# Optimization experiments

Hardware: AMD Instinct MI355X
Metric: run time of the kernel (lower is better)

The kernel has to match this reference:

```python
import jax, jax.numpy as jnp
import numpy as np

NUM_GROUPS = 32
EPS = 1e-6
NUM_HEADS = 8
HEAD_DIM = 64


def group_norm(x, gamma, beta):
    # x: [B, C, H, W]
    B, C, H, W = x.shape
    xg = x.reshape(B, NUM_GROUPS, C // NUM_GROUPS, H, W)
    mean = xg.mean(axis=(2, 3, 4), keepdims=True)
    var = xg.var(axis=(2, 3, 4), keepdims=True)
    xn = ((xg - mean) * jax.lax.rsqrt(var + EPS)).reshape(B, C, H, W)
    return xn * gamma[None, :, None, None] + beta[None, :, None, None]


def setup_inputs() -> dict:
    key = jax.random.key(0)
    ks = jax.random.split(key, 4)
    B, C, H, W = 8, 512, 32, 32
    hid = NUM_HEADS * HEAD_DIM  # 512
    x = jax.random.normal(ks[0], (B, C, H, W), dtype=jnp.float32)
    gamma = jnp.ones((C,), dtype=jnp.float32)
    beta = jnp.zeros((C,), dtype=jnp.float32)
    w_in = jax.random.normal(ks[1], (3 * hid, C), dtype=jnp.float32) * (1.0 / np.sqrt(C))
    b_in = jnp.zeros((3 * hid,), dtype=jnp.float32)
    w_out = jax.random.normal(ks[2], (C, hid), dtype=jnp.float32) * (1.0 / np.sqrt(hid))
    b_out = jnp.zeros((C,), dtype=jnp.float32)
    return {"x": x, "gamma": gamma, "beta": beta, "w_in": w_in, "b_in": b_in,
            "w_out": w_out, "b_out": b_out}


def reference(x, gamma, beta, w_in, b_in, w_out, b_out):
    B, C, H, W = x.shape
    n, c = NUM_HEADS, HEAD_DIM
    skip = x
    h = group_norm(x, gamma, beta)
    # 1x1 conv proj_in: [B, 3*n*c, H, W]
    qkv = jnp.einsum('oc,bchw->bohw', w_in, h) + b_in[None, :, None, None]
    qkv = qkv.reshape(B, 3, n, c, H * W)
    q, k, v = qkv[:, 0], qkv[:, 1], qkv[:, 2]  # each [B, n, c, HW]
    scale = 1.0 / np.sqrt(c)
    logits = jnp.einsum('bncq,bnck->bnqk', q, k) * scale  # [B, n, HW, HW]
    w = jax.nn.softmax(logits, axis=-1)
    out = jnp.einsum('bnqk,bnck->bncq', w, v)  # [B, n, c, HW]
    out = out.reshape(B, n * c, H, W)
    out = jnp.einsum('oc,bchw->bohw', w_out, out) + b_out[None, :, None, None]
    return out + skip
```

## Files before the change

### kernel.cpp

```cpp
#include <hip/hip_runtime.h>
#include <hip/hip_bf16.h>

#define B_    8
#define C_    512
#define HW_   1024
#define NG    32
#define GCH   16
#define EPSV  1e-6f

typedef __attribute__((ext_vector_type(8))) short short8;
typedef __attribute__((ext_vector_type(4))) short short4v;
typedef __attribute__((ext_vector_type(4))) float floatx4;

static __device__ __forceinline__ short f2bs(float f) {
  return __builtin_bit_cast(short, __float2bfloat16(f));
}
static __device__ __forceinline__ short4v pack4(float a, float b, float c, float d) {
  return (short4v){f2bs(a), f2bs(b), f2bs(c), f2bs(d)};
}
#define MFMA(a, b, c) __builtin_amdgcn_mfma_f32_16x16x32_bf16((a), (b), (c), 0, 0, 0)

static __device__ __forceinline__ void glds16(const short* g, short* l) {
  __builtin_amdgcn_global_load_lds(
      (const __attribute__((address_space(1))) void*)g,
      (__attribute__((address_space(3))) void*)l, 16, 0, 0);
}

__global__ __launch_bounds__(256) void cast2_f2b(
    const float* __restrict__ s1, short* __restrict__ d1,
    const float* __restrict__ s2, short* __restrict__ d2) {
  int i = blockIdx.x * 256 + threadIdx.x;
  const float* s; short* d; int j;
  if (i < 196608) { s = s1; d = d1; j = i; }
  else            { s = s2; d = d2; j = i - 196608; }
  float4 v = reinterpret_cast<const float4*>(s)[j];
  reinterpret_cast<short4v*>(d)[j] = pack4(v.x, v.y, v.z, v.w);
}

__global__ __launch_bounds__(256) void gn_stats(
    const float* __restrict__ x, float2* __restrict__ stats) {
  int bg = blockIdx.x;
  const int n = GCH * HW_;
  const float* xp = x + (size_t)bg * n;
  int t = threadIdx.x;

  float s = 0.f, ss = 0.f;
  for (int i = t; i < n / 4; i += 256) {
    float4 v = *reinterpret_cast<const float4*>(xp + i * 4);
    s  += (v.x + v.y) + (v.z + v.w);
    ss += (v.x * v.x + v.y * v.y) + (v.z * v.z + v.w * v.w);
  }
  for (int o = 32; o > 0; o >>= 1) {
    s  += __shfl_down(s, o);
    ss += __shfl_down(ss, o);
  }
  __shared__ float rs_[4], rss_[4];
  int wid = t >> 6, lane = t & 63;
  if (lane == 0) { rs_[wid] = s; rss_[wid] = ss; }
  __syncthreads();
  if (t == 0) {
    float stot  = rs_[0] + rs_[1] + rs_[2] + rs_[3];
    float sstot = rss_[0] + rss_[1] + rss_[2] + rss_[3];
    float mean = stot / (float)n;
    float var  = sstot / (float)n - mean * mean;
    stats[bg] = make_float2(mean, rsqrtf(var + EPSV));
  }
}

__global__ __launch_bounds__(256) void gn_apply(
    const float* __restrict__ x, const float2* __restrict__ stats,
    const float* __restrict__ gamma, const float* __restrict__ beta,
    short* __restrict__ ht) {
  __shared__ float Ls[64 * 65];
  int s0 = blockIdx.x * 64, ch0 = blockIdx.y * 64, b = blockIdx.z;
  int t = threadIdx.x;

  for (int i = 0; i < 4; i++) {
    int lin = t + i * 256;
    int r = lin >> 4, c4 = lin & 15;
    int ch = ch0 + r;
    float2 st = stats[b * NG + (ch >> 4)];
    float ga = gamma[ch] * st.y;
    float be = beta[ch] - st.x * ga;
    float4 v = *reinterpret_cast<const float4*>(
        x + ((size_t)(b * C_ + ch)) * HW_ + s0 + c4 * 4);
    Ls[r * 65 + c4 * 4 + 0] = v.x * ga + be;
    Ls[r * 65 + c4 * 4 + 1] = v.y * ga + be;
    Ls[r * 65 + c4 * 4 + 2] = v.z * ga + be;
    Ls[r * 65 + c4 * 4 + 3] = v.w * ga + be;
  }
  __syncthreads();
  for (int i = 0; i < 4; i++) {
    int lin = t + i * 256;
    int sq = lin >> 4, cq = lin & 15;
    float a0 = Ls[(cq * 4 + 0) * 65 + sq];
    float a1 = Ls[(cq * 4 + 1) * 65 + sq];
    float a2 = Ls[(cq * 4 + 2) * 65 + sq];
    float a3 = Ls[(cq * 4 + 3) * 65 + sq];
    *reinterpret_cast<short4v*>(
        ht + ((size_t)b * 1024 + s0 + sq) * 512 + ch0 + cq * 4) =
        pack4(a0, a1, a2, a3);
  }
}

__global__ __launch_bounds__(256) void gemm_qkv(
    const short* __restrict__ Wb, const short* __restrict__ ht,
    const float* __restrict__ bias,
    short* __restrict__ Qt, short* __restrict__ Kt, short* __restrict__ Vn) {
  __shared__ short As[2][4096];
  __shared__ short Bs[2][4096];
  int bx = blockIdx.x, by = blockIdx.y, bb = blockIdx.z;
  int m0 = by * 128, n0 = bx * 128;
  int t = threadIdx.x;
  int w = t >> 6, lane = t & 63, n16 = lane & 15, quad = lane >> 4;
  int wm = (w >> 1) * 64, wn = (w & 1) * 64;

  const short* Wa = Wb + (size_t)(m0 + (t >> 2)) * 512 + (t & 3) * 8;
  const short* Xa = ht + (size_t)bb * 1024 * 512 +
                    (size_t)(n0 + (t >> 2)) * 512 + (t & 3) * 8;

#define STAGE(buf, kk)                                                \
  do {                                                                \
    glds16(Wa + (kk), &As[buf][t * 8]);                               \
    glds16(Wa + 64 * 512 + (kk), &As[buf][2048 + t * 8]);             \
    glds16(Xa + (kk), &Bs[buf][t * 8]);                               \
    glds16(Xa + 64 * 512 + (kk), &Bs[buf][2048 + t * 8]);             \
  } while (0)

  floatx4 acc[4][4];
  for (int i = 0; i < 4; i++)
    for (int j = 0; j < 4; j++) acc[i][j] = (floatx4){0.f, 0.f, 0.f, 0.f};

  STAGE(0, 0);
#pragma unroll 1
  for (int ks = 0; ks < 16; ks++) {
    int cur = ks & 1;
    __syncthreads();
    if (ks < 15) STAGE(cur ^ 1, (ks + 1) * 32);
    short8 a[4], b[4];
    for (int im = 0; im < 4; im++)
      a[im] = *reinterpret_cast<const short8*>(
          &As[cur][(wm + im * 16 + n16) * 32 + quad * 8]);
    for (int in = 0; in < 4; in++)
      b[in] = *reinterpret_cast<const short8*>(
          &Bs[cur][(wn + in * 16 + n16) * 32 + quad * 8]);
    for (int im = 0; im < 4; im++)
      for (int in = 0; in < 4; in++)
        acc[im][in] = MFMA(a[im], b[in], acc[im][in]);
  }
#undef STAGE

  if (m0 < 1024) {
    const bool isQ = (m0 < 512);
    short* base = isQ ? Qt : Kt;
    const float sc = isQ ? 0.125f : 1.0f;
    for (int im = 0; im < 4; im++) {
      int m = m0 + wm + im * 16 + quad * 4;
      int hh = (m >> 6) & 7, d0 = m & 63;
      float4 bi = *reinterpret_cast<const float4*>(&bias[m]);
      short* hb = base + (size_t)(bb * 8 + hh) * 1024 * 64 + d0;
      for (int in = 0; in < 4; in++) {
        int nn = n0 + wn + in * 16 + n16;
        *reinterpret_cast<short4v*>(hb + (size_t)nn * 64) =
            pack4((acc[im][in][0] + bi.x) * sc, (acc[im][in][1] + bi.y) * sc,
                  (acc[im][in][2] + bi.z) * sc, (acc[im][in][3] + bi.w) * sc);
      }
    }
  } else {
    for (int im = 0; im < 4; im++) {
      int m = m0 + wm + im * 16 + quad * 4;
      float4 bi = *reinterpret_cast<const float4*>(&bias[m]);
      int ch = m - 1024;
      for (int in = 0; in < 4; in++) {
        int nn = n0 + wn + in * 16 + n16;
        short* vp = Vn + (size_t)(bb * 512 + ch) * 1024 + nn;
        vp[0]    = f2bs(acc[im][in][0] + bi.x);
        vp[1024] = f2bs(acc[im][in][1] + bi.y);
        vp[2048] = f2bs(acc[im][in][2] + bi.z);
        vp[3072] = f2bs(acc[im][in][3] + bi.w);
      }
    }
  }
}

__global__ __launch_bounds__(256, 2) void attn_mfma(
    const short* __restrict__ Qt, const short* __restrict__ Kt,
    const short* __restrict__ Vn, short* __restrict__ attnT) {
  __shared__ short Ps[4][2][2][1024];
  int blk0 = blockIdx.x;
  int blk = (blk0 & 7) * 64 + (blk0 >> 3);
  int qb = blk & 7, h = (blk >> 3) & 7, b = blk >> 6;
  int t = threadIdx.x;
  int w = t >> 6, lane = t & 63, n16 = lane & 15, quad = lane >> 4;
  int q0 = qb * 128 + w * 32;

  const short* Qp = Qt + (size_t)(b * 8 + h) * 1024 * 64;
  const short* Kp = Kt + (size_t)(b * 8 + h) * 1024 * 64;
  const short* Vp = Vn + (size_t)(b * 512 + h * 64) * 1024;

  short8 qa[2][2];
  for (int qt = 0; qt < 2; qt++)
    for (int f = 0; f < 2; f++)
      qa[qt][f] = *reinterpret_cast<const short8*>(
          Qp + (size_t)(q0 + qt * 16 + n16) * 64 + f * 32 + quad * 8);

  floatx4 O[2][4];
  float l[2][4];
  for (int qt = 0; qt < 2; qt++)
    for (int i = 0; i < 4; i++) {
      O[qt][i] = (floatx4){0.f, 0.f, 0.f, 0.f};
      l[qt][i] = 0.f;
    }

#define LOADK(dst, ktv)                                                      \
  do {                                                                       \
    int k0_ = (ktv) * 64;                                                    \
    for (int nt_ = 0; nt_ < 4; nt_++)                                        \
      for (int f_ = 0; f_ < 2; f_++)                                         \
        dst[nt_][f_] = *reinterpret_cast<const short8*>(                     \
            Kp + (size_t)(k0_ + nt_ * 16 + n16) * 64 + f_ * 32 + quad * 8);  \
  } while (0)

#define BODY(kf, ktv)                                                        \
  do {                                                                       \
    int k0_ = (ktv) * 64;                                                    \
    floatx4 S0_[4], S1_[4];                                                  \
    for (int nt_ = 0; nt_ < 4; nt_++) {                                      \
      floatx4 sa_ = (floatx4){0.f, 0.f, 0.f, 0.f};                           \
      sa_ = MFMA(qa[0][0], kf[nt_][0], sa_);                                 \
      S0_[nt_] = MFMA(qa[0][1], kf[nt_][1], sa_);                            \
    }                                                                        \
    for (int nt_ = 0; nt_ < 4; nt_++) {                                      \
      floatx4 sa_ = (floatx4){0.f, 0.f, 0.f, 0.f};                           \
      sa_ = MFMA(qa[1][0], kf[nt_][0], sa_);                                 \
      S1_[nt_] = MFMA(qa[1][1], kf[nt_][1], sa_);                            \
    }                                                                        \
        \
    short8 v_[4][2];                                                         \
    for (int nd_ = 0; nd_ < 4; nd_++) {                                      \
      const short* vs_ =                                                     \
          Vp + (size_t)(nd_ * 16 + n16) * 1024 + k0_ + quad * 8;             \
      v_[nd_][0] = *reinterpret_cast<const short8*>(vs_);                    \
      v_[nd_][1] = *reinterpret_cast<const short8*>(vs_ + 32);               \
    }                                                                        \
    short* Pb_ = &Ps[w][(ktv) & 1][0][0];                                    \
    int sub_ = n16 & 7, hi_ = n16 >> 3;                                      \
    for (int r_ = 0; r_ < 4; r_++) {                                         \
      int row_ = quad * 4 + r_;                                              \
      float p0_ = __expf(S0_[0][r_]);                                        \
      float p1_ = __expf(S0_[1][r_]);                                        \
      float p2_ = __expf(S0_[2][r_]);                                        \
      float p3_ = __expf(S0_[3][r_]);                                        \
      l[0][r_] += (p0_ + p1_) + (p2_ + p3_);                                 \
      Pb_[row_ * 64 + ((0 + hi_ + row_) & 7) * 8 + sub_] = f2bs(p0_);        \
      Pb_[row_ * 64 + ((2 + hi_ + row_) & 7) * 8 + sub_] = f2bs(p1_);        \
      Pb_[row_ * 64 + ((4 + hi_ + row_) & 7) * 8 + sub_] = f2bs(p2_);        \
      Pb_[row_ * 64 + ((6 + hi_ + row_) & 7) * 8 + sub_] = f2bs(p3_);        \
    }                                                                        \
    for (int r_ = 0; r_ < 4; r_++) {                                         \
      int row_ = quad * 4 + r_;                                              \
      float p0_ = __expf(S1_[0][r_]);                                        \
      float p1_ = __expf(S1_[1][r_]);                                        \
      float p2_ = __expf(S1_[2][r_]);                                        \
      float p3_ = __expf(S1_[3][r_]);                                        \
      l[1][r_] += (p0_ + p1_) + (p2_ + p3_);                                 \
      Pb_[1024 + row_ * 64 + ((0 + hi_ + row_) & 7) * 8 + sub_] = f2bs(p0_); \
      Pb_[1024 + row_ * 64 + ((2 + hi_ + row_) & 7) * 8 + sub_] = f2bs(p1_); \
      Pb_[1024 + row_ * 64 + ((4 + hi_ + row_) & 7) * 8 + sub_] = f2bs(p2_); \
      Pb_[1024 + row_ * 64 + ((6 + hi_ + row_) & 7) * 8 + sub_] = f2bs(p3_); \
    }                                                                        \
    short8 pa0_[2], pa1_[2];                                                 \
    for (int f_ = 0; f_ < 2; f_++) {                                         \
      pa0_[f_] = *reinterpret_cast<const short8*>(                           \
          Pb_ + n16 * 64 + ((quad + 4 * f_ + n16) & 7) * 8);                 \
      pa1_[f_] = *reinterpret_cast<const short8*>(                           \
          Pb_ + 1024 + n16 * 64 + ((quad + 4 * f_ + n16) & 7) * 8);          \
    }                                                                        \
    __builtin_amdgcn_s_setprio(1);                                           \
    for (int nd_ = 0; nd_ < 4; nd_++) {                                      \
      O[0][nd_] = MFMA(pa0_[0], v_[nd_][0], O[0][nd_]);                      \
      O[0][nd_] = MFMA(pa0_[1], v_[nd_][1], O[0][nd_]);                      \
      O[1][nd_] = MFMA(pa1_[0], v_[nd_][0], O[1][nd_]);                      \
      O[1][nd_] = MFMA(pa1_[1], v_[nd_][1], O[1][nd_]);                      \
    }                                                                        \
    __builtin_amdgcn_s_setprio(0);                                           \
  } while (0)

  short8 kfA[4][2], kfB[4][2];
  LOADK(kfA, 0);
#pragma unroll 1
  for (int kt = 0; kt < 16; kt += 2) {
    LOADK(kfB, kt + 1);
    BODY(kfA, kt);
    if (kt + 2 < 16) LOADK(kfA, kt + 2);
    BODY(kfB, kt + 1);
  }
#undef LOADK
#undef BODY

  for (int qt = 0; qt < 2; qt++)
    for (int r = 0; r < 4; r++) {
      float s = l[qt][r];
      s += __shfl_xor(s, 1);
      s += __shfl_xor(s, 2);
      s += __shfl_xor(s, 4);
      s += __shfl_xor(s, 8);
      l[qt][r] = 1.0f / s;
    }
  for (int qt = 0; qt < 2; qt++)
    for (int nd = 0; nd < 4; nd++)
      for (int r = 0; r < 4; r++) {
        int q = q0 + qt * 16 + quad * 4 + r;
        int ch = h * 64 + nd * 16 + n16;
        attnT[((size_t)b * 1024 + q) * 512 + ch] = f2bs(O[qt][nd][r] * l[qt][r]);
      }
}

__global__ __launch_bounds__(256) void gemm_out(
    const short* __restrict__ Wb, const short* __restrict__ Xt,
    const float* __restrict__ bias, const float* __restrict__ resid,
    float* __restrict__ out) {
  __shared__ short As[2][4096];
  __shared__ short Bs[2][4096];
  int bx = blockIdx.x, by = blockIdx.y, bb = blockIdx.z;
  int m0 = by * 128, n0 = bx * 128;
  int t = threadIdx.x;
  int w = t >> 6, lane = t & 63, n16 = lane & 15, quad = lane >> 4;
  int wm = (w >> 1) * 64, wn = (w & 1) * 64;

  const short* Wa = Wb + (size_t)(m0 + (t >> 2)) * 512 + (t & 3) * 8;
  const short* Xa = Xt + (size_t)bb * 1024 * 512 +
                    (size_t)(n0 + (t >> 2)) * 512 + (t & 3) * 8;

#define STAGE(buf, kk)                                                \
  do {                                                                \
    glds16(Wa + (kk), &As[buf][t * 8]);                               \
    glds16(Wa + 64 * 512 + (kk), &As[buf][2048 + t * 8]);             \
    glds16(Xa + (kk), &Bs[buf][t * 8]);                               \
    glds16(Xa + 64 * 512 + (kk), &Bs[buf][2048 + t * 8]);             \
  } while (0)

  floatx4 acc[4][4];
  for (int i = 0; i < 4; i++)
    for (int j = 0; j < 4; j++) acc[i][j] = (floatx4){0.f, 0.f, 0.f, 0.f};

  STAGE(0, 0);
#pragma unroll 1
  for (int ks = 0; ks < 16; ks++) {
    int cur = ks & 1;
    __syncthreads();
    if (ks < 15) STAGE(cur ^ 1, (ks + 1) * 32);
    short8 a[4], b[4];
    for (int im = 0; im < 4; im++)
      a[im] = *reinterpret_cast<const short8*>(
          &As[cur][(wm + im * 16 + n16) * 32 + quad * 8]);
    for (int in = 0; in < 4; in++)
      b[in] = *reinterpret_cast<const short8*>(
          &Bs[cur][(wn + in * 16 + n16) * 32 + quad * 8]);
    for (int im = 0; im < 4; im++)
      for (int in = 0; in < 4; in++)
        acc[im][in] = MFMA(a[im], b[in], acc[im][in]);
  }
#undef STAGE

  for (int im = 0; im < 4; im++) {
    int m = m0 + wm + im * 16 + quad * 4;
    float4 bi = *reinterpret_cast<const float4*>(&bias[m]);
    for (int in = 0; in < 4; in++) {
      int nn = n0 + wn + in * 16 + n16;
      size_t idx = ((size_t)bb * 512 + m) * 1024 + nn;
      out[idx]        = acc[im][in][0] + bi.x + resid[idx];
      out[idx + 1024] = acc[im][in][1] + bi.y + resid[idx + 1024];
      out[idx + 2048] = acc[im][in][2] + bi.z + resid[idx + 2048];
      out[idx + 3072] = acc[im][in][3] + bi.w + resid[idx + 3072];
    }
  }
}

extern "C" void kernel_launch(void* const* d_in, const int* in_sizes, int n_in,
                              void* d_out, int out_size, void* d_ws, size_t ws_size,
                              hipStream_t stream) {
  const float* x     = (const float*)d_in[0];
  const float* gamma = (const float*)d_in[1];
  const float* beta  = (const float*)d_in[2];
  const float* w_in  = (const float*)d_in[3];
  const float* b_in  = (const float*)d_in[4];
  const float* w_out = (const float*)d_in[5];
  const float* b_out = (const float*)d_in[6];
  float* out = (float*)d_out;

  char* ws = (char*)d_ws;
  short* ht    = (short*)ws;
  short* Qt    = (short*)(ws + (8u  << 20));
  short* Kt    = (short*)(ws + (16u << 20));
  short* Vn    = (short*)(ws + (24u << 20));
  short* attnT = (short*)(ws + (32u << 20));
  short* wbf1  = (short*)(ws + (40u << 20));
  short* wbf2  = (short*)(ws + (42u << 20));
  float2* stats = (float2*)(ws + (44u << 20));

  cast2_f2b<<<1024, 256, 0, stream>>>(w_in, wbf1, w_out, wbf2);
  gn_stats<<<B_ * NG, 256, 0, stream>>>(x, stats);
  gn_apply<<<dim3(16, 8, B_), 256, 0, stream>>>(x, stats, gamma, beta, ht);
  gemm_qkv<<<dim3(8, 12, B_), 256, 0, stream>>>(wbf1, ht, b_in, Qt, Kt, Vn);
  attn_mfma<<<B_ * 8 * 8, 256, 0, stream>>>(Qt, Kt, Vn, attnT);
  gemm_out<<<dim3(8, 4, B_), 256, 0, stream>>>(wbf2, attnT, b_out, x, out);
}
```

Measured before the change: 193.4 us.

## Split attention over key range with reduce kernel and shrink output GEMM tiles

Attention blocks now process half of the key tiles each, writing unnormalized fp32 partial outputs and row sums to workspace. A new reduce kernel combines them and normalizes into bf16. The output GEMM uses 64x64 tiles instead of 128x128 to launch more blocks. Together these raise parallelism on the many-CU GPU, at the cost of extra workspace traffic, an extra launch, and less data reuse in the GEMM. The split is enabled only when the workspace is large enough.

```diff
diff --git a/kernel.cpp b/kernel.cpp
--- a/kernel.cpp
+++ b/kernel.cpp
@@ -185,11 +185,14 @@
 
 __global__ __launch_bounds__(256, 2) void attn_mfma(
     const short* __restrict__ Qt, const short* __restrict__ Kt,
-    const short* __restrict__ Vn, short* __restrict__ attnT) {
+    const short* __restrict__ Vn, short* __restrict__ attnT,
+    float* __restrict__ Opart, float* __restrict__ lpart, int ksplit) {
   __shared__ short Ps[4][2][2][1024];
+  int nblk = gridDim.x;
   int blk0 = blockIdx.x;
-  int blk = (blk0 & 7) * 64 + (blk0 >> 3);
-  int qb = blk & 7, h = (blk >> 3) & 7, b = blk >> 6;
+  int blk = (blk0 & 7) * (nblk >> 3) + (blk0 >> 3);
+  int tile = blk / ksplit, split = blk % ksplit;
+  int qb = tile & 7, h = (tile >> 3) & 7, b = tile >> 6;
   int t = threadIdx.x;
   int w = t >> 6, lane = t & 63, n16 = lane & 15, quad = lane >> 4;
   int q0 = qb * 128 + w * 32;
@@ -286,13 +289,15 @@
     __builtin_amdgcn_s_setprio(0);                                           \
   } while (0)
 
+  int ktn = 16 / ksplit;
+  int kt0 = split * ktn, ktend = kt0 + ktn;
   short8 kfA[4][2], kfB[4][2];
-  LOADK(kfA, 0);
+  LOADK(kfA, kt0);
 #pragma unroll 1
-  for (int kt = 0; kt < 16; kt += 2) {
+  for (int kt = kt0; kt < ktend; kt += 2) {
     LOADK(kfB, kt + 1);
     BODY(kfA, kt);
-    if (kt + 2 < 16) LOADK(kfA, kt + 2);
+    if (kt + 2 < ktend) LOADK(kfA, kt + 2);
     BODY(kfB, kt + 1);
   }
 #undef LOADK
@@ -305,28 +310,67 @@
       s += __shfl_xor(s, 2);
       s += __shfl_xor(s, 4);
       s += __shfl_xor(s, 8);
-      l[qt][r] = 1.0f / s;
+      l[qt][r] = s;
     }
-  for (int qt = 0; qt < 2; qt++)
-    for (int nd = 0; nd < 4; nd++)
-      for (int r = 0; r < 4; r++) {
-        int q = q0 + qt * 16 + quad * 4 + r;
-        int ch = h * 64 + nd * 16 + n16;
-        attnT[((size_t)b * 1024 + q) * 512 + ch] = f2bs(O[qt][nd][r] * l[qt][r]);
-      }
+
+  if (ksplit == 1) {
+    for (int qt = 0; qt < 2; qt++)
+      for (int nd = 0; nd < 4; nd++)
+        for (int r = 0; r < 4; r++) {
+          int q = q0 + qt * 16 + quad * 4 + r;
+          int ch = h * 64 + nd * 16 + n16;
+          attnT[((size_t)b * 1024 + q) * 512 + ch] =
+              f2bs(O[qt][nd][r] / l[qt][r]);
+        }
+  } else {
+    float* Ob = Opart + (size_t)blk * 8192;
+    float* lb = lpart + blk * 128;
+    int ql0 = w * 32;
+    for (int qt = 0; qt < 2; qt++)
+      for (int r = 0; r < 4; r++)
+        if (n16 == 0) lb[ql0 + qt * 16 + quad * 4 + r] = l[qt][r];
+    for (int qt = 0; qt < 2; qt++)
+      for (int nd = 0; nd < 4; nd++)
+        for (int r = 0; r < 4; r++)
+          Ob[(ql0 + qt * 16 + quad * 4 + r) * 64 + nd * 16 + n16] =
+              O[qt][nd][r];
+  }
+}
+
+__global__ __launch_bounds__(256) void attn_reduce(
+    const float* __restrict__ Opart, const float* __restrict__ lpart,
+    short* __restrict__ attnT) {
+  int j0 = blockIdx.x;
+  int j = (j0 & 7) * 64 + (j0 >> 3);
+  int t = threadIdx.x;
+  int b = j >> 6, h = (j >> 3) & 7, qb = j & 7;
+  const float4* O0 = reinterpret_cast<const float4*>(
+      Opart + (size_t)(j * 2) * 8192);
+  const float* l0 = lpart + (j * 2) * 128;
+  for (int i = 0; i < 8; i++) {
+    int lin = i * 256 + t;
+    int q = lin >> 4, d4 = lin & 15;
+    float4 a = O0[lin];
+    float4 c = O0[2048 + lin];
+    float inv = 1.0f / (l0[q] + l0[128 + q]);
+    *reinterpret_cast<short4v*>(
+        attnT + ((size_t)(b * 1024 + qb * 128 + q)) * 512 + h * 64 + d4 * 4) =
+        pack4((a.x + c.x) * inv, (a.y + c.y) * inv,
+              (a.z + c.z) * inv, (a.w + c.w) * inv);
+  }
 }
 
 __global__ __launch_bounds__(256) void gemm_out(
     const short* __restrict__ Wb, const short* __restrict__ Xt,
     const float* __restrict__ bias, const float* __restrict__ resid,
     float* __restrict__ out) {
-  __shared__ short As[2][4096];
-  __shared__ short Bs[2][4096];
+  __shared__ short As[2][2048];
+  __shared__ short Bs[2][2048];
   int bx = blockIdx.x, by = blockIdx.y, bb = blockIdx.z;
-  int m0 = by * 128, n0 = bx * 128;
+  int m0 = by * 64, n0 = bx * 64;
   int t = threadIdx.x;
   int w = t >> 6, lane = t & 63, n16 = lane & 15, quad = lane >> 4;
-  int wm = (w >> 1) * 64, wn = (w & 1) * 64;
+  int wm = (w >> 1) * 32, wn = (w & 1) * 32;
 
   const short* Wa = Wb + (size_t)(m0 + (t >> 2)) * 512 + (t & 3) * 8;
   const short* Xa = Xt + (size_t)bb * 1024 * 512 +
@@ -335,14 +379,12 @@
 #define STAGE(buf, kk)                                                \
   do {                                                                \
     glds16(Wa + (kk), &As[buf][t * 8]);                               \
-    glds16(Wa + 64 * 512 + (kk), &As[buf][2048 + t * 8]);             \
     glds16(Xa + (kk), &Bs[buf][t * 8]);                               \
-    glds16(Xa + 64 * 512 + (kk), &Bs[buf][2048 + t * 8]);             \
   } while (0)
 
-  floatx4 acc[4][4];
-  for (int i = 0; i < 4; i++)
-    for (int j = 0; j < 4; j++) acc[i][j] = (floatx4){0.f, 0.f, 0.f, 0.f};
+  floatx4 acc[2][2];
+  for (int i = 0; i < 2; i++)
+    for (int j = 0; j < 2; j++) acc[i][j] = (floatx4){0.f, 0.f, 0.f, 0.f};
 
   STAGE(0, 0);
 #pragma unroll 1
@@ -350,23 +392,23 @@
     int cur = ks & 1;
     __syncthreads();
     if (ks < 15) STAGE(cur ^ 1, (ks + 1) * 32);
-    short8 a[4], b[4];
-    for (int im = 0; im < 4; im++)
+    short8 a[2], b[2];
+    for (int im = 0; im < 2; im++)
       a[im] = *reinterpret_cast<const short8*>(
           &As[cur][(wm + im * 16 + n16) * 32 + quad * 8]);
-    for (int in = 0; in < 4; in++)
+    for (int in = 0; in < 2; in++)
       b[in] = *reinterpret_cast<const short8*>(
           &Bs[cur][(wn + in * 16 + n16) * 32 + quad * 8]);
-    for (int im = 0; im < 4; im++)
-      for (int in = 0; in < 4; in++)
+    for (int im = 0; im < 2; im++)
+      for (int in = 0; in < 2; in++)
         acc[im][in] = MFMA(a[im], b[in], acc[im][in]);
   }
 #undef STAGE
 
-  for (int im = 0; im < 4; im++) {
+  for (int im = 0; im < 2; im++) {
     int m = m0 + wm + im * 16 + quad * 4;
     float4 bi = *reinterpret_cast<const float4*>(&bias[m]);
-    for (int in = 0; in < 4; in++) {
+    for (int in = 0; in < 2; in++) {
       int nn = n0 + wn + in * 16 + n16;
       size_t idx = ((size_t)bb * 512 + m) * 1024 + nn;
       out[idx]        = acc[im][in][0] + bi.x + resid[idx];
@@ -398,11 +440,18 @@
   short* wbf1  = (short*)(ws + (40u << 20));
   short* wbf2  = (short*)(ws + (42u << 20));
   float2* stats = (float2*)(ws + (44u << 20));
+  float* Opart = (float*)(ws + (46u << 20));
+  float* lpart = (float*)(ws + (80u << 20));
+
+  int ksplit = (ws_size >= ((size_t)81 << 20)) ? 2 : 1;
 
   cast2_f2b<<<1024, 256, 0, stream>>>(w_in, wbf1, w_out, wbf2);
   gn_stats<<<B_ * NG, 256, 0, stream>>>(x, stats);
   gn_apply<<<dim3(16, 8, B_), 256, 0, stream>>>(x, stats, gamma, beta, ht);
   gemm_qkv<<<dim3(8, 12, B_), 256, 0, stream>>>(wbf1, ht, b_in, Qt, Kt, Vn);
-  attn_mfma<<<B_ * 8 * 8, 256, 0, stream>>>(Qt, Kt, Vn, attnT);
-  gemm_out<<<dim3(8, 4, B_), 256, 0, stream>>>(wbf2, attnT, b_out, x, out);
-}
+  attn_mfma<<<512 * ksplit, 256, 0, stream>>>(Qt, Kt, Vn, attnT, Opart, lpart,
+                                              ksplit);
+  if (ksplit == 2)
+    attn_reduce<<<512, 256, 0, stream>>>(Opart, lpart, attnT);
+  gemm_out<<<dim3(16, 8, B_), 256, 0, stream>>>(wbf2, attnT, b_out, x, out);
+}
```

New measurement: 199.4 us. 3.1% more time.

## Transpose QK^T MFMA and shuffle P in registers; shrink gemm_out tiles

Applied to the files above, without the earlier changes.

The attention kernel now computes S^T (K as A operand) so each lane holds probabilities for one query column, and the P matrix is repacked into MFMA A-operand layout with cross-lane shuffles instead of going through LDS. The row-sum bookkeeping is reduced to one accumulator per q-tile and the occupancy hint is dropped. Separately, gemm_out switches from 128x128 to 64x64 tiles, launching four times more blocks to fill the GPU better. The changes trade LDS traffic for shuffle instructions and give up some per-block data reuse in gemm_out.

```diff
diff --git a/kernel.cpp b/kernel.cpp
--- a/kernel.cpp
+++ b/kernel.cpp
@@ -17,6 +17,10 @@
 }
 static __device__ __forceinline__ short4v pack4(float a, float b, float c, float d) {
   return (short4v){f2bs(a), f2bs(b), f2bs(c), f2bs(d)};
+}
+static __device__ __forceinline__ unsigned pk2(float a, float b) {
+  return (unsigned)(unsigned short)f2bs(a) |
+         ((unsigned)(unsigned short)f2bs(b) << 16);
 }
 #define MFMA(a, b, c) __builtin_amdgcn_mfma_f32_16x16x32_bf16((a), (b), (c), 0, 0, 0)
 
@@ -183,16 +187,18 @@
   }
 }
 
-__global__ __launch_bounds__(256, 2) void attn_mfma(
+__global__ __launch_bounds__(256) void attn_mfma(
     const short* __restrict__ Qt, const short* __restrict__ Kt,
     const short* __restrict__ Vn, short* __restrict__ attnT) {
-  __shared__ short Ps[4][2][2][1024];
   int blk0 = blockIdx.x;
   int blk = (blk0 & 7) * 64 + (blk0 >> 3);
   int qb = blk & 7, h = (blk >> 3) & 7, b = blk >> 6;
   int t = threadIdx.x;
   int w = t >> 6, lane = t & 63, n16 = lane & 15, quad = lane >> 4;
   int q0 = qb * 128 + w * 32;
+  int qhi = quad >> 1;
+  int srcA = ((quad & 1) << 5) + n16;
+  int srcB = srcA + 16;
 
   const short* Qp = Qt + (size_t)(b * 8 + h) * 1024 * 64;
   const short* Kp = Kt + (size_t)(b * 8 + h) * 1024 * 64;
@@ -205,12 +211,9 @@
           Qp + (size_t)(q0 + qt * 16 + n16) * 64 + f * 32 + quad * 8);
 
   floatx4 O[2][4];
-  float l[2][4];
+  float l[2] = {0.f, 0.f};
   for (int qt = 0; qt < 2; qt++)
-    for (int i = 0; i < 4; i++) {
-      O[qt][i] = (floatx4){0.f, 0.f, 0.f, 0.f};
-      l[qt][i] = 0.f;
-    }
+    for (int i = 0; i < 4; i++) O[qt][i] = (floatx4){0.f, 0.f, 0.f, 0.f};
 
 #define LOADK(dst, ktv)                                                      \
   do {                                                                       \
@@ -224,18 +227,7 @@
 #define BODY(kf, ktv)                                                        \
   do {                                                                       \
     int k0_ = (ktv) * 64;                                                    \
-    floatx4 S0_[4], S1_[4];                                                  \
-    for (int nt_ = 0; nt_ < 4; nt_++) {                                      \
-      floatx4 sa_ = (floatx4){0.f, 0.f, 0.f, 0.f};                           \
-      sa_ = MFMA(qa[0][0], kf[nt_][0], sa_);                                 \
-      S0_[nt_] = MFMA(qa[0][1], kf[nt_][1], sa_);                            \
-    }                                                                        \
-    for (int nt_ = 0; nt_ < 4; nt_++) {                                      \
-      floatx4 sa_ = (floatx4){0.f, 0.f, 0.f, 0.f};                           \
-      sa_ = MFMA(qa[1][0], kf[nt_][0], sa_);                                 \
-      S1_[nt_] = MFMA(qa[1][1], kf[nt_][1], sa_);                            \
-    }                                                                        \
-        \
+      \
     short8 v_[4][2];                                                         \
     for (int nd_ = 0; nd_ < 4; nd_++) {                                      \
       const short* vs_ =                                                     \
@@ -243,47 +235,54 @@
       v_[nd_][0] = *reinterpret_cast<const short8*>(vs_);                    \
       v_[nd_][1] = *reinterpret_cast<const short8*>(vs_ + 32);               \
     }                                                                        \
-    short* Pb_ = &Ps[w][(ktv) & 1][0][0];                                    \
-    int sub_ = n16 & 7, hi_ = n16 >> 3;                                      \
-    for (int r_ = 0; r_ < 4; r_++) {                                         \
-      int row_ = quad * 4 + r_;                                              \
-      float p0_ = __expf(S0_[0][r_]);                                        \
-      float p1_ = __expf(S0_[1][r_]);                                        \
-      float p2_ = __expf(S0_[2][r_]);                                        \
-      float p3_ = __expf(S0_[3][r_]);                                        \
-      l[0][r_] += (p0_ + p1_) + (p2_ + p3_);                                 \
-      Pb_[row_ * 64 + ((0 + hi_ + row_) & 7) * 8 + sub_] = f2bs(p0_);        \
-      Pb_[row_ * 64 + ((2 + hi_ + row_) & 7) * 8 + sub_] = f2bs(p1_);        \
-      Pb_[row_ * 64 + ((4 + hi_ + row_) & 7) * 8 + sub_] = f2bs(p2_);        \
-      Pb_[row_ * 64 + ((6 + hi_ + row_) & 7) * 8 + sub_] = f2bs(p3_);        \
+    _Pragma("unroll")                                                        \
+    for (int qt_ = 0; qt_ < 2; qt_++) {                                      \
+               \
+      floatx4 T_[4];                                                         \
+      _Pragma("unroll")                                                      \
+      for (int nt_ = 0; nt_ < 4; nt_++) {                                    \
+        floatx4 s_ = (floatx4){0.f, 0.f, 0.f, 0.f};                          \
+        s_ = MFMA(kf[nt_][0], qa[qt_][0], s_);                               \
+        T_[nt_] = MFMA(kf[nt_][1], qa[qt_][1], s_);                          \
+      }                                                                      \
+      unsigned u_[4][2];                                                     \
+      _Pragma("unroll")                                                      \
+      for (int nt_ = 0; nt_ < 4; nt_++) {                                    \
+        float p0_ = __expf(T_[nt_][0]);                                      \
+        float p1_ = __expf(T_[nt_][1]);                                      \
+        float p2_ = __expf(T_[nt_][2]);                                      \
+        float p3_ = __expf(T_[nt_][3]);                                      \
+        l[qt_] += (p0_ + p1_) + (p2_ + p3_);                                 \
+        u_[nt_][0] = pk2(p0_, p1_);                                         \
+        u_[nt_][1] = pk2(p2_, p3_);                                         \
+      }                                                                      \
+                         \
+      short8 pa_[2];                                                         \
+      _Pragma("unroll")                                                      \
+      for (int f_ = 0; f_ < 2; f_++) {                                       \
+        unsigned a0_ = (unsigned)__shfl((int)u_[2 * f_ + 0][0], srcA);       \
+        unsigned a1_ = (unsigned)__shfl((int)u_[2 * f_ + 1][0], srcA);       \
+        unsigned b0_ = (unsigned)__shfl((int)u_[2 * f_ + 0][1], srcA);       \
+        unsigned b1_ = (unsigned)__shfl((int)u_[2 * f_ + 1][1], srcA);       \
+        unsigned c0_ = (unsigned)__shfl((int)u_[2 * f_ + 0][0], srcB);       \
+        unsigned c1_ = (unsigned)__shfl((int)u_[2 * f_ + 1][0], srcB);       \
+        unsigned d0_ = (unsigned)__shfl((int)u_[2 * f_ + 0][1], srcB);       \
+        unsigned d1_ = (unsigned)__shfl((int)u_[2 * f_ + 1][1], srcB);       \
+        uint4 wv_;                                                           \
+        wv_.x = qhi ? a1_ : a0_;                                             \
+        wv_.y = qhi ? b1_ : b0_;                                             \
+        wv_.z = qhi ? c1_ : c0_;                                             \
+        wv_.w = qhi ? d1_ : d0_;                                             \
+        pa_[f_] = __builtin_bit_cast(short8, wv_);                           \
+      }                                                                      \
+      __builtin_amdgcn_s_setprio(1);                                         \
+      _Pragma("unroll")                                                      \
+      for (int nd_ = 0; nd_ < 4; nd_++) {                                    \
+        O[qt_][nd_] = MFMA(pa_[0], v_[nd_][0], O[qt_][nd_]);                 \
+        O[qt_][nd_] = MFMA(pa_[1], v_[nd_][1], O[qt_][nd_]);                 \
+      }                                                                      \
+      __builtin_amdgcn_s_setprio(0);                                         \
     }                                                                        \
-    for (int r_ = 0; r_ < 4; r_++) {                                         \
-      int row_ = quad * 4 + r_;                                              \
-      float p0_ = __expf(S1_[0][r_]);                                        \
-      float p1_ = __expf(S1_[1][r_]);                                        \
-      float p2_ = __expf(S1_[2][r_]);                                        \
-      float p3_ = __expf(S1_[3][r_]);                                        \
-      l[1][r_] += (p0_ + p1_) + (p2_ + p3_);                                 \
-      Pb_[1024 + row_ * 64 + ((0 + hi_ + row_) & 7) * 8 + sub_] = f2bs(p0_); \
-      Pb_[1024 + row_ * 64 + ((2 + hi_ + row_) & 7) * 8 + sub_] = f2bs(p1_); \
-      Pb_[1024 + row_ * 64 + ((4 + hi_ + row_) & 7) * 8 + sub_] = f2bs(p2_); \
-      Pb_[1024 + row_ * 64 + ((6 + hi_ + row_) & 7) * 8 + sub_] = f2bs(p3_); \
-    }                                                                        \
-    short8 pa0_[2], pa1_[2];                                                 \
-    for (int f_ = 0; f_ < 2; f_++) {                                         \
-      pa0_[f_] = *reinterpret_cast<const short8*>(                           \
-          Pb_ + n16 * 64 + ((quad + 4 * f_ + n16) & 7) * 8);                 \
-      pa1_[f_] = *reinterpret_cast<const short8*>(                           \
-          Pb_ + 1024 + n16 * 64 + ((quad + 4 * f_ + n16) & 7) * 8);          \
-    }                                                                        \
-    __builtin_amdgcn_s_setprio(1);                                           \
-    for (int nd_ = 0; nd_ < 4; nd_++) {                                      \
-      O[0][nd_] = MFMA(pa0_[0], v_[nd_][0], O[0][nd_]);                      \
-      O[0][nd_] = MFMA(pa0_[1], v_[nd_][1], O[0][nd_]);                      \
-      O[1][nd_] = MFMA(pa1_[0], v_[nd_][0], O[1][nd_]);                      \
-      O[1][nd_] = MFMA(pa1_[1], v_[nd_][1], O[1][nd_]);                      \
-    }                                                                        \
-    __builtin_amdgcn_s_setprio(0);                                           \
   } while (0)
 
   short8 kfA[4][2], kfB[4][2];
@@ -298,35 +297,31 @@
 #undef LOADK
 #undef BODY
 
-  for (int qt = 0; qt < 2; qt++)
-    for (int r = 0; r < 4; r++) {
-      float s = l[qt][r];
-      s += __shfl_xor(s, 1);
-      s += __shfl_xor(s, 2);
-      s += __shfl_xor(s, 4);
-      s += __shfl_xor(s, 8);
-      l[qt][r] = 1.0f / s;
-    }
-  for (int qt = 0; qt < 2; qt++)
+  for (int qt = 0; qt < 2; qt++) {
+    float s = l[qt];
+    s += __shfl_xor(s, 16);
+    s += __shfl_xor(s, 32);
     for (int nd = 0; nd < 4; nd++)
       for (int r = 0; r < 4; r++) {
+        float linv = 1.0f / __shfl(s, quad * 4 + r);
         int q = q0 + qt * 16 + quad * 4 + r;
         int ch = h * 64 + nd * 16 + n16;
-        attnT[((size_t)b * 1024 + q) * 512 + ch] = f2bs(O[qt][nd][r] * l[qt][r]);
+        attnT[((size_t)b * 1024 + q) * 512 + ch] = f2bs(O[qt][nd][r] * linv);
       }
+  }
 }
 
 __global__ __launch_bounds__(256) void gemm_out(
     const short* __restrict__ Wb, const short* __restrict__ Xt,
     const float* __restrict__ bias, const float* __restrict__ resid,
     float* __restrict__ out) {
-  __shared__ short As[2][4096];
-  __shared__ short Bs[2][4096];
+  __shared__ short As[2][2048];
+  __shared__ short Bs[2][2048];
   int bx = blockIdx.x, by = blockIdx.y, bb = blockIdx.z;
-  int m0 = by * 128, n0 = bx * 128;
+  int m0 = by * 64, n0 = bx * 64;
   int t = threadIdx.x;
   int w = t >> 6, lane = t & 63, n16 = lane & 15, quad = lane >> 4;
-  int wm = (w >> 1) * 64, wn = (w & 1) * 64;
+  int wm = (w >> 1) * 32, wn = (w & 1) * 32;
 
   const short* Wa = Wb + (size_t)(m0 + (t >> 2)) * 512 + (t & 3) * 8;
   const short* Xa = Xt + (size_t)bb * 1024 * 512 +
@@ -335,14 +330,12 @@
 #define STAGE(buf, kk)                                                \
   do {                                                                \
     glds16(Wa + (kk), &As[buf][t * 8]);                               \
-    glds16(Wa + 64 * 512 + (kk), &As[buf][2048 + t * 8]);             \
     glds16(Xa + (kk), &Bs[buf][t * 8]);                               \
-    glds16(Xa + 64 * 512 + (kk), &Bs[buf][2048 + t * 8]);             \
   } while (0)
 
-  floatx4 acc[4][4];
-  for (int i = 0; i < 4; i++)
-    for (int j = 0; j < 4; j++) acc[i][j] = (floatx4){0.f, 0.f, 0.f, 0.f};
+  floatx4 acc[2][2];
+  for (int i = 0; i < 2; i++)
+    for (int j = 0; j < 2; j++) acc[i][j] = (floatx4){0.f, 0.f, 0.f, 0.f};
 
   STAGE(0, 0);
 #pragma unroll 1
@@ -350,23 +343,23 @@
     int cur = ks & 1;
     __syncthreads();
     if (ks < 15) STAGE(cur ^ 1, (ks + 1) * 32);
-    short8 a[4], b[4];
-    for (int im = 0; im < 4; im++)
+    short8 a[2], b[2];
+    for (int im = 0; im < 2; im++)
       a[im] = *reinterpret_cast<const short8*>(
           &As[cur][(wm + im * 16 + n16) * 32 + quad * 8]);
-    for (int in = 0; in < 4; in++)
+    for (int in = 0; in < 2; in++)
       b[in] = *reinterpret_cast<const short8*>(
           &Bs[cur][(wn + in * 16 + n16) * 32 + quad * 8]);
-    for (int im = 0; im < 4; im++)
-      for (int in = 0; in < 4; in++)
+    for (int im = 0; im < 2; im++)
+      for (int in = 0; in < 2; in++)
         acc[im][in] = MFMA(a[im], b[in], acc[im][in]);
   }
 #undef STAGE
 
-  for (int im = 0; im < 4; im++) {
+  for (int im = 0; im < 2; im++) {
     int m = m0 + wm + im * 16 + quad * 4;
     float4 bi = *reinterpret_cast<const float4*>(&bias[m]);
-    for (int in = 0; in < 4; in++) {
+    for (int in = 0; in < 2; in++) {
       int nn = n0 + wn + in * 16 + n16;
       size_t idx = ((size_t)bb * 512 + m) * 1024 + nn;
       out[idx]        = acc[im][in][0] + bi.x + resid[idx];
@@ -403,6 +396,6 @@
   gn_stats<<<B_ * NG, 256, 0, stream>>>(x, stats);
   gn_apply<<<dim3(16, 8, B_), 256, 0, stream>>>(x, stats, gamma, beta, ht);
   gemm_qkv<<<dim3(8, 12, B_), 256, 0, stream>>>(wbf1, ht, b_in, Qt, Kt, Vn);
-  attn_mfma<<<B_ * 8 * 8, 256, 0, stream>>>(Qt, Kt, Vn, attnT);
-  gemm_out<<<dim3(8, 4, B_), 256, 0, stream>>>(wbf2, attnT, b_out, x, out);
-}
+  attn_mfma<<<512, 256, 0, stream>>>(Qt, Kt, Vn, attnT);
+  gemm_out<<<dim3(16, 8, B_), 256, 0, stream>>>(wbf2, attnT, b_out, x, out);
+}
```

Result: no change. 191.7 us (-0.9%).
